# Kernel optimization log

Hardware: AMD Instinct MI355X
Metric: run time of the kernel (lower is better)

The kernel has to match this reference:

```python
import jax, jax.numpy as jnp
import numpy as np

B, S, HID = 2, 2048, 2048
H, D = 16, 128
BASE = 10000.0
NEG = -1e9


def _rope_tables(seq_len, dim, dtype):
    inv_freq = 1.0 / (BASE ** (jnp.arange(0, dim, 2, dtype=jnp.float32) / dim))
    pos = jnp.arange(seq_len, dtype=jnp.float32)
    freqs = jnp.einsum('s,d->sd', pos, inv_freq)          # [S, D/2]
    emb = jnp.concatenate([freqs, freqs], axis=-1)        # [S, D]
    return jnp.cos(emb).astype(dtype), jnp.sin(emb).astype(dtype)


def _rotate_half(x):
    x1, x2 = jnp.split(x, 2, axis=-1)
    return jnp.concatenate([-x2, x1], axis=-1)


def setup_inputs() -> dict:
    key = jax.random.key(0)
    k1, k2, k3 = jax.random.split(key, 3)
    x = jax.random.normal(k1, (B, S, HID), dtype=jnp.float32)
    w_qkv = jax.random.normal(k2, (HID, 3 * HID), dtype=jnp.float32) * (HID ** -0.5)
    w_out = jax.random.normal(k3, (HID, HID), dtype=jnp.float32) * (HID ** -0.5)
    return {"x": x, "w_qkv": w_qkv, "w_out": w_out}


def reference(x, w_qkv, w_out):
    b, s, _ = x.shape
    qkv = x @ w_qkv                                        # [B, S, 3*HID]
    qkv = qkv.reshape(b, s, 3, H, D).transpose(2, 0, 3, 1, 4)  # [3, B, H, S, D]
    q, k, v = qkv[0], qkv[1], qkv[2]
    cos, sin = _rope_tables(s, D, x.dtype)                 # [S, D]
    cos = cos[None, None]
    sin = sin[None, None]
    q = q * cos + _rotate_half(q) * sin
    k = k * cos + _rotate_half(k) * sin
    scale = 1.0 / np.sqrt(D)
    scores = jnp.einsum('bhqd,bhkd->bhqk', q, k) * scale   # [B, H, S, S]
    causal = jnp.triu(jnp.ones((s, s), dtype=bool), k=1)
    scores = jnp.where(causal[None, None], NEG, scores)
    attn = jax.nn.softmax(scores, axis=-1)
    out = jnp.einsum('bhqk,bhkd->bhqd', attn, v)           # [B, H, S, D]
    out = out.transpose(0, 2, 1, 3).reshape(b, s, H * D)
    return out @ w_out
```

## Files before the change

kernel.cpp:

```cpp
#include <hip/hip_runtime.h>
#include <hip/hip_bf16.h>

#define S_LEN 2048
#define HID_DIM 2048
#define NH 16
#define HD 128
#define N3 6144

typedef __bf16 bf16x8 __attribute__((ext_vector_type(8)));
typedef float f32x4 __attribute__((ext_vector_type(4)));
typedef float f32x16 __attribute__((ext_vector_type(16)));

#define MFMA16(a, b, c) __builtin_amdgcn_mfma_f32_16x16x32_bf16(a, b, c, 0, 0, 0)
#define MFMA32(a, b, c) __builtin_amdgcn_mfma_f32_32x32x16_bf16(a, b, c, 0, 0, 0)

__device__ __forceinline__ unsigned short f2bf(float f) {
  union { float f; unsigned u; } v; v.f = f;
  return (unsigned short)((v.u + 0x7fffu + ((v.u >> 16) & 1u)) >> 16);
}
__device__ __forceinline__ float bf2f(unsigned short h) {
  union { unsigned u; float f; } v; v.u = ((unsigned)h) << 16; return v.f;
}
__device__ __forceinline__ unsigned packbf2(float lo, float hi) {
  union { __hip_bfloat162 h2; unsigned u; } cv;
  cv.h2 = __float22bfloat162_rn(make_float2(lo, hi));
  return cv.u;
}
__device__ __forceinline__ void store_c(float* p, float v) { *p = v; }
__device__ __forceinline__ void store_c(unsigned short* p, float v) { *p = f2bf(v); }

__device__ __forceinline__ void async16(const void* g, void* l) {
  __builtin_amdgcn_global_load_lds((const __attribute__((address_space(1))) unsigned int*)g,
                                   (__attribute__((address_space(3))) unsigned int*)l,
                                   16, 0, 0);
}

__global__ __launch_bounds__(256) void cast_bf16(const float4* __restrict__ src,
                                                 ushort4* __restrict__ dst) {
  int i = blockIdx.x * 256 + threadIdx.x;
  float4 v = src[i];
  ushort4 o;
  o.x = f2bf(v.x); o.y = f2bf(v.y); o.z = f2bf(v.z); o.w = f2bf(v.w);
  dst[i] = o;
}

__global__ __launch_bounds__(256) void transpose_cast(const float* __restrict__ src,
                                                      unsigned short* __restrict__ dst,
                                                      int R, int Ccols) {
  __shared__ float t[32][33];
  int ct = Ccols >> 5;
  int bx = blockIdx.x % ct, by = blockIdx.x / ct;
  int c0 = bx << 5, r0 = by << 5;
  int lx = threadIdx.x & 31, ly = threadIdx.x >> 5;
#pragma unroll
  for (int i = 0; i < 32; i += 8)
    t[ly + i][lx] = src[(long long)(r0 + ly + i) * Ccols + c0 + lx];
  __syncthreads();
#pragma unroll
  for (int i = 0; i < 32; i += 8)
    dst[(long long)(c0 + ly + i) * R + r0 + lx] = f2bf(t[lx][ly + i]);
}

__global__ __launch_bounds__(256) void rope_tables(float* __restrict__ cosT,
                                                   float* __restrict__ sinT) {
  int idx = blockIdx.x * 256 + threadIdx.x;
  int s = idx >> 6, i = idx & 63;
  float invf = powf(10000.0f, -(float)i * (1.0f / 64.0f));
  float a = (float)s * invf;
  cosT[idx] = cosf(a);
  sinT[idx] = sinf(a);
}

template <int BM, int BN, int WM, int WN, typename OutT>
__global__ __launch_bounds__(512) void gemm_pipe(const unsigned short* __restrict__ A,
                                                 const unsigned short* __restrict__ Bt,
                                                 OutT* __restrict__ C,
                                                 int Mdim, int Ndim, int Kdim) {
  constexpr int WTM = BM / WM, WTN = BN / WN;
  constexpr int MREP = WTM / 16, NREP = WTN / 16;
  constexpr int AEL = BM * 64;
  constexpr int BEL = BN * 64;
  constexpr int BUFE = AEL + BEL;
  __shared__ unsigned short smem[2 * BUFE];

  const int ntn = Ndim / BN;
  const int nwg = (Mdim / BM) * ntn;
  int bid = blockIdx.x;
  bid = (bid & 7) * (nwg >> 3) + (bid >> 3);
  const int tm = (bid / ntn) * BM;
  const int tn = (bid % ntn) * BN;

  const int tid = threadIdx.x;
  const int w = tid >> 6, l = tid & 63;
  const int g = l >> 4, cc = l & 15;
  const int wm = w / WN, wn = w % WN;

  const int srow = tid >> 3;
  const int schunk = (tid & 7) ^ (srow & 7);
  const unsigned short* gA = A + (long long)(tm + srow) * Kdim + schunk * 8;
  const unsigned short* gB = Bt + (long long)(tn + srow) * Kdim + schunk * 8;

  const int ch0 = ((g) ^ (cc & 7)) << 3;
  const int ch1 = ((4 + g) ^ (cc & 7)) << 3;

  f32x4 acc[MREP][NREP] = {};
  bf16x8 a[MREP / 2][2], b[NREP][2];

  const int nk = Kdim >> 6;

#pragma unroll
  for (int s = 0; s < BM / 64; ++s)
    async16(gA + (long long)s * 64 * Kdim, smem + s * 4096 + w * 512);
#pragma unroll
  for (int s = 0; s < BN / 64; ++s)
    async16(gB + (long long)s * 64 * Kdim, smem + AEL + s * 4096 + w * 512);
  asm volatile("s_waitcnt vmcnt(0)" ::: "memory");
  __builtin_amdgcn_s_barrier();

  for (int kt = 0; kt < nk; ++kt) {
    const int buf = kt & 1;
    const unsigned short* Ab = smem + buf * BUFE + (wm * WTM) * 64;
    const unsigned short* Bb = smem + buf * BUFE + AEL + (wn * WTN) * 64;
    const long long kb = (long long)(kt + 1) << 6;
    unsigned short* nb = smem + (buf ^ 1) * BUFE;

#pragma unroll
    for (int i = 0; i < MREP / 2; ++i) {
      const int r = (i * 16 + cc) << 6;
      a[i][0] = *(const bf16x8*)(Ab + r + ch0);
      a[i][1] = *(const bf16x8*)(Ab + r + ch1);
    }
#pragma unroll
    for (int j = 0; j < NREP; ++j) {
      const int r = (j * 16 + cc) << 6;
      b[j][0] = *(const bf16x8*)(Bb + r + ch0);
      b[j][1] = *(const bf16x8*)(Bb + r + ch1);
    }
    if (kt + 1 < nk) {
#pragma unroll
      for (int s = 0; s < BM / 64; ++s)
        async16(gA + (long long)s * 64 * Kdim + kb, nb + s * 4096 + w * 512);
    }
    __builtin_amdgcn_s_barrier();
    __builtin_amdgcn_s_setprio(1);
#pragma unroll
    for (int i = 0; i < MREP / 2; ++i)
#pragma unroll
      for (int j = 0; j < NREP / 2; ++j) {
        acc[i][j] = MFMA16(a[i][0], b[j][0], acc[i][j]);
        acc[i][j] = MFMA16(a[i][1], b[j][1], acc[i][j]);
      }
    __builtin_amdgcn_s_setprio(0);
    __builtin_amdgcn_s_barrier();

    if (kt + 1 < nk) {
#pragma unroll
      for (int s = 0; s < BN / 64; ++s)
        async16(gB + (long long)s * 64 * Kdim + kb, nb + AEL + s * 4096 + w * 512);
    }
    __builtin_amdgcn_s_barrier();
    __builtin_amdgcn_s_setprio(1);
#pragma unroll
    for (int i = 0; i < MREP / 2; ++i)
#pragma unroll
      for (int j = 0; j < NREP / 2; ++j) {
        acc[i][NREP / 2 + j] = MFMA16(a[i][0], b[NREP / 2 + j][0], acc[i][NREP / 2 + j]);
        acc[i][NREP / 2 + j] = MFMA16(a[i][1], b[NREP / 2 + j][1], acc[i][NREP / 2 + j]);
      }
    __builtin_amdgcn_s_setprio(0);
    __builtin_amdgcn_s_barrier();

#pragma unroll
    for (int i = 0; i < MREP / 2; ++i) {
      const int r = ((WTM / 2) + i * 16 + cc) << 6;
      a[i][0] = *(const bf16x8*)(Ab + r + ch0);
      a[i][1] = *(const bf16x8*)(Ab + r + ch1);
    }
    __builtin_amdgcn_s_barrier();
    __builtin_amdgcn_s_setprio(1);
#pragma unroll
    for (int i = 0; i < MREP / 2; ++i)
#pragma unroll
      for (int j = 0; j < NREP / 2; ++j) {
        acc[MREP / 2 + i][j] = MFMA16(a[i][0], b[j][0], acc[MREP / 2 + i][j]);
        acc[MREP / 2 + i][j] = MFMA16(a[i][1], b[j][1], acc[MREP / 2 + i][j]);
      }
    __builtin_amdgcn_s_setprio(0);
    __builtin_amdgcn_s_barrier();

    __builtin_amdgcn_s_setprio(1);
#pragma unroll
    for (int i = 0; i < MREP / 2; ++i)
#pragma unroll
      for (int j = 0; j < NREP / 2; ++j) {
        acc[MREP / 2 + i][NREP / 2 + j] =
            MFMA16(a[i][0], b[NREP / 2 + j][0], acc[MREP / 2 + i][NREP / 2 + j]);
        acc[MREP / 2 + i][NREP / 2 + j] =
            MFMA16(a[i][1], b[NREP / 2 + j][1], acc[MREP / 2 + i][NREP / 2 + j]);
      }
    __builtin_amdgcn_s_setprio(0);
    asm volatile("s_waitcnt vmcnt(0)" ::: "memory");
    __builtin_amdgcn_s_barrier();
  }

  const int crow0 = tm + wm * WTM;
  const int ccol0 = tn + wn * WTN;
#pragma unroll
  for (int i = 0; i < MREP; ++i)
#pragma unroll
    for (int j = 0; j < NREP; ++j)
#pragma unroll
      for (int p = 0; p < 4; ++p) {
        int row = crow0 + i * 16 + (g << 2) + p;
        int col = ccol0 + j * 16 + cc;
        store_c(&C[(long long)row * Ndim + col], acc[i][j][p]);
      }
}

__global__ __launch_bounds__(256) void split_rope(const unsigned short* __restrict__ qkv,
                                                  const float* __restrict__ cosT,
                                                  const float* __restrict__ sinT,
                                                  unsigned short* __restrict__ Qb,
                                                  unsigned short* __restrict__ Kb,
                                                  unsigned short* __restrict__ Vt) {
  __shared__ unsigned short vtile[32][128];
  const int bid = blockIdx.x;
  const int st = bid & 63;
  const int h = (bid >> 6) & 15;
  const int b = bid >> 10;
  const int s0 = st << 5;
  const int t = threadIdx.x;
  const int d = t & 127;
  const int sl0 = t >> 7;
  const int dh = d & 63;
  const float sgn = (d < 64) ? -1.0f : 1.0f;
  const float qscale = 0.08838834764831845f;
#pragma unroll
  for (int it = 0; it < 16; ++it) {
    const int sl = sl0 + (it << 1);
    const int s = s0 + sl;
    const long long rb = ((long long)(b * S_LEN + s)) * N3 + h * HD;
    const float cv = cosT[(s << 6) + dh];
    const float sv = sinT[(s << 6) + dh];
    float qv = bf2f(qkv[rb + d]);
    float qo = bf2f(qkv[rb + (d ^ 64)]);
    float kv = bf2f(qkv[rb + HID_DIM + d]);
    float ko = bf2f(qkv[rb + HID_DIM + (d ^ 64)]);
    const long long ob = ((long long)((b * NH + h) * S_LEN + s)) * HD + d;
    Qb[ob] = f2bf((qv * cv + sgn * qo * sv) * qscale);
    Kb[ob] = f2bf(kv * cv + sgn * ko * sv);
    vtile[sl][d] = qkv[rb + 2 * HID_DIM + d];
  }
  __syncthreads();
  const int dr = t >> 1;
  const int sh = (t & 1) << 4;
  unsigned short tv[16];
#pragma unroll
  for (int j = 0; j < 16; ++j) tv[j] = vtile[sh + j][dr];
  uint4 u0, u1;
  u0.x = (unsigned)tv[0] | ((unsigned)tv[1] << 16);
  u0.y = (unsigned)tv[2] | ((unsigned)tv[3] << 16);
  u0.z = (unsigned)tv[4] | ((unsigned)tv[5] << 16);
  u0.w = (unsigned)tv[6] | ((unsigned)tv[7] << 16);
  u1.x = (unsigned)tv[8] | ((unsigned)tv[9] << 16);
  u1.y = (unsigned)tv[10] | ((unsigned)tv[11] << 16);
  u1.z = (unsigned)tv[12] | ((unsigned)tv[13] << 16);
  u1.w = (unsigned)tv[14] | ((unsigned)tv[15] << 16);
  const long long vb = ((long long)((b * NH + h) * HD + dr)) * S_LEN + s0 + sh;
  *(uint4*)(Vt + vb) = u0;
  *(uint4*)(Vt + vb + 8) = u1;
}

__global__ __launch_bounds__(256) void flash_attn(const unsigned short* __restrict__ Qg,
                                                  const unsigned short* __restrict__ Kg,
                                                  const unsigned short* __restrict__ Vt,
                                                  unsigned short* __restrict__ Ob) {
  __shared__ unsigned short smem[32768];
  const int id = blockIdx.x;
  const int bh = id & 31;
  const int qtr = (id >> 5) & 7;
  const int qt = (id >> 8) ? qtr : 15 - qtr;
  const int Q0 = qt << 7;
  const int b = bh >> 4, h = bh & 15;
  const long long base = (long long)bh * (S_LEN * HD);
  const int tid = threadIdx.x, w = tid >> 6, l = tid & 63;
  const int hi = l >> 5, q = l & 31;
  const int q0w = Q0 + (w << 5);
  const int g = l >> 4, c = l & 15;

  bf16x8 qf[8];
  {
    const unsigned short* qp = Qg + base + (long long)(q0w + q) * HD + (hi << 3);
#pragma unroll
    for (int s = 0; s < 8; ++s) qf[s] = *(const bf16x8*)(qp + (s << 4));
  }

  f32x16 oacc[4] = {};
  float m = -1e30f, lsum = 0.f;

  const int nt = (qt << 1) + 2;

  auto STAGE = [&](int kv0, int buf) {
    unsigned short* ks = smem + buf * 8192;
    unsigned short* vs = smem + 16384 + buf * 8192;
#pragma unroll
    for (int j = 0; j < 4; ++j) {
      int row = (w << 4) + (j << 2) + g;
      int chunk = c ^ (row & 7);
      async16(Kg + base + (long long)(kv0 + row) * HD + (chunk << 3),
              ks + (((w << 4) + (j << 2)) << 7));
    }
#pragma unroll
    for (int j = 0; j < 4; ++j) {
      int dr = (w << 5) + (j << 3) + (l >> 3);
      int chunk = (l & 7) ^ (dr & 7);
      async16(Vt + base + (long long)dr * S_LEN + kv0 + (chunk << 3),
              vs + (((w << 5) + (j << 3)) << 6));
    }
  };

  STAGE(0, 0);
  __syncthreads();

  int cur = 0;
  for (int t = 0; t < nt; ++t) {
    const int kv0 = t << 6;
    if (t + 1 < nt) STAGE((t + 1) << 6, cur ^ 1);

    if (kv0 < q0w + 32) {
      const unsigned short* ks = smem + cur * 8192;
      const unsigned short* vs = smem + 16384 + cur * 8192;

      f32x16 sa[2] = {};
#pragma unroll
      for (int h2 = 0; h2 < 2; ++h2) {
        const char* kb = (const char*)ks + (((h2 << 5) + q) << 8);
        const int r7 = q & 7;
#pragma unroll
        for (int s = 0; s < 8; ++s) {
          bf16x8 kf = *(const bf16x8*)(kb + ((((s << 1) + hi) ^ r7) << 4));
          sa[h2] = MFMA32(kf, qf[s], sa[h2]);
        }
      }

      if (kv0 + 63 > q0w) {
        const int qq = q0w + q;
#pragma unroll
        for (int h2 = 0; h2 < 2; ++h2)
#pragma unroll
          for (int j = 0; j < 16; ++j) {
            int kv = kv0 + (h2 << 5) + (j & 3) + ((j >> 2) << 3) + (hi << 2);
            if (kv > qq) sa[h2][j] = -1e30f;
          }
      }

      float tmax = -1e30f;
#pragma unroll
      for (int h2 = 0; h2 < 2; ++h2)
#pragma unroll
        for (int j = 0; j < 16; ++j) tmax = fmaxf(tmax, sa[h2][j]);
      tmax = fmaxf(tmax, __shfl_xor(tmax, 32));
      float mn = fmaxf(m, tmax);
      float fsc = __expf(m - mn);
      m = mn;
      float ps = 0.f;
#pragma unroll
      for (int h2 = 0; h2 < 2; ++h2)
#pragma unroll
        for (int j = 0; j < 16; ++j) {
          float pv = __expf(sa[h2][j] - mn);
          sa[h2][j] = pv;
          ps += pv;
        }
      ps += __shfl_xor(ps, 32);
      lsum = lsum * fsc + ps;
#pragma unroll
      for (int db = 0; db < 4; ++db)
#pragma unroll
        for (int j = 0; j < 16; ++j) oacc[db][j] *= fsc;

      unsigned up[2][8], wp[2][8];
#pragma unroll
      for (int h2 = 0; h2 < 2; ++h2)
#pragma unroll
        for (int k = 0; k < 8; ++k)
          up[h2][k] = packbf2(sa[h2][2 * k], sa[h2][2 * k + 1]);
#pragma unroll
      for (int h2 = 0; h2 < 2; ++h2)
#pragma unroll
        for (int k = 0; k < 8; ++k)
          wp[h2][k] = __shfl_xor((int)up[h2][k], 32);
      union Frag { unsigned u[4]; bf16x8 v; } pf[4];
#pragma unroll
      for (int s = 0; s < 4; ++s) {
        int h2 = s >> 1, q4 = (s & 1) << 2;
        pf[s].u[0] = hi ? wp[h2][q4 + 2] : up[h2][q4];
        pf[s].u[1] = hi ? wp[h2][q4 + 3] : up[h2][q4 + 1];
        pf[s].u[2] = hi ? up[h2][q4 + 2] : wp[h2][q4];
        pf[s].u[3] = hi ? up[h2][q4 + 3] : wp[h2][q4 + 1];
      }

#pragma unroll
      for (int db = 0; db < 4; ++db) {
        const char* vb = (const char*)vs + (((db << 5) + q) << 7);
        const int d7 = q & 7;
#pragma unroll
        for (int s = 0; s < 4; ++s) {
          bf16x8 vf = *(const bf16x8*)(vb + ((((s << 1) + hi) ^ d7) << 4));
          oacc[db] = MFMA32(vf, pf[s].v, oacc[db]);
        }
      }
    }

    __syncthreads();
    cur ^= 1;
  }

  const float rl = 1.0f / lsum;
#pragma unroll
  for (int db = 0; db < 4; ++db)
#pragma unroll
    for (int jg = 0; jg < 4; ++jg) {
      int d = (db << 5) + (jg << 3) + (hi << 2);
      unsigned v0 = packbf2(oacc[db][4 * jg] * rl, oacc[db][4 * jg + 1] * rl);
      unsigned v1 = packbf2(oacc[db][4 * jg + 2] * rl, oacc[db][4 * jg + 3] * rl);
      *(uint2*)(smem + (((w << 5) + q) << 7) + d) = make_uint2(v0, v1);
    }
  __syncthreads();
  {
    const int qr = tid >> 1;
    const int dh = (tid & 1) << 6;
    const uint4* src = (const uint4*)(smem + (qr << 7) + dh);
    uint4* dst = (uint4*)(Ob + (long long)((b << 11) + Q0 + qr) * HID_DIM + (h << 7) + dh);
#pragma unroll
    for (int cc2 = 0; cc2 < 8; ++cc2) dst[cc2] = src[cc2];
  }
}

extern "C" void kernel_launch(void* const* d_in, const int* in_sizes, int n_in,
                              void* d_out, int out_size, void* d_ws, size_t ws_size,
                              hipStream_t stream) {
  (void)in_sizes; (void)n_in; (void)out_size; (void)ws_size;
  const float* x = (const float*)d_in[0];
  const float* w_qkv = (const float*)d_in[1];
  const float* w_out = (const float*)d_in[2];
  float* out = (float*)d_out;
  char* ws = (char*)d_ws;

  unsigned short* xb    = (unsigned short*)(ws);
  unsigned short* wqkvT = (unsigned short*)(ws + 16777216);
  unsigned short* woutT = (unsigned short*)(ws + 41943040);
  unsigned short* qkv   = (unsigned short*)(ws + 50331648);
  unsigned short* Qb    = (unsigned short*)(ws + 100663296);
  unsigned short* Kb    = (unsigned short*)(ws + 117440512);
  unsigned short* Vt    = (unsigned short*)(ws + 134217728);
  float* cosT = (float*)(ws + 150994944);
  float* sinT = (float*)(ws + 151519232);
  unsigned short* Ob = qkv;

  cast_bf16<<<8192, 256, 0, stream>>>((const float4*)x, (ushort4*)xb);
  transpose_cast<<<12288, 256, 0, stream>>>(w_qkv, wqkvT, 2048, 6144);
  transpose_cast<<<4096, 256, 0, stream>>>(w_out, woutT, 2048, 2048);
  rope_tables<<<512, 256, 0, stream>>>(cosT, sinT);
  gemm_pipe<256, 256, 2, 4, unsigned short><<<384, 512, 0, stream>>>(xb, wqkvT, qkv, 4096, 6144, 2048);
  split_rope<<<2048, 256, 0, stream>>>(qkv, cosT, sinT, Qb, Kb, Vt);
  flash_attn<<<512, 256, 0, stream>>>(Qb, Kb, Vt, Ob);
  gemm_pipe<256, 128, 4, 2, float><<<256, 512, 0, stream>>>(Ob, woutT, out, 4096, 2048, 2048);
}
```

Before: 297.2 us.

## Deepen GEMM prefetch pipeline with split staging and partial vmcnt waits

Restructures the double-buffered GEMM so loads for tile k+2 are issued in halves interleaved between MFMA phases, and the loop waits with a partial vmcnt instead of draining all outstanding loads. This is meant to keep global-to-LDS transfers in flight across iterations and hide memory latency. The output projection GEMM also switches from a 256x128 tile with a 4x2 warp grid to a 128x256 tile with a fixed 2x4 grid. The design depends on exact vmcnt counts matching the number of issued instructions, and on correct buffer reuse ordering, which adds correctness risk.

```diff
diff --git a/kernel.cpp b/kernel.cpp
--- a/kernel.cpp
+++ b/kernel.cpp
@@ -34,6 +34,11 @@
                                    (__attribute__((address_space(3))) unsigned int*)l,
                                    16, 0, 0);
 }
+
+template <int N> __device__ __forceinline__ void vmcnt();
+template <> __device__ __forceinline__ void vmcnt<0>() { asm volatile("s_waitcnt vmcnt(0)" ::: "memory"); }
+template <> __device__ __forceinline__ void vmcnt<5>() { asm volatile("s_waitcnt vmcnt(5)" ::: "memory"); }
+template <> __device__ __forceinline__ void vmcnt<6>() { asm volatile("s_waitcnt vmcnt(6)" ::: "memory"); }
 
 __global__ __launch_bounds__(256) void cast_bf16(const float4* __restrict__ src,
                                                  ushort4* __restrict__ dst) {
@@ -71,16 +76,17 @@
   sinT[idx] = sinf(a);
 }
 
-template <int BM, int BN, int WM, int WN, typename OutT>
-__global__ __launch_bounds__(512) void gemm_pipe(const unsigned short* __restrict__ A,
-                                                 const unsigned short* __restrict__ Bt,
-                                                 OutT* __restrict__ C,
-                                                 int Mdim, int Ndim, int Kdim) {
-  constexpr int WTM = BM / WM, WTN = BN / WN;
+template <int BM, int BN, typename OutT>
+__global__ __launch_bounds__(512) void gemm_pipe8(const unsigned short* __restrict__ A,
+                                                  const unsigned short* __restrict__ Bt,
+                                                  OutT* __restrict__ C,
+                                                  int Mdim, int Ndim, int Kdim) {
+  constexpr int WTM = BM / 2, WTN = BN / 4;
   constexpr int MREP = WTM / 16, NREP = WTN / 16;
-  constexpr int AEL = BM * 64;
-  constexpr int BEL = BN * 64;
-  constexpr int BUFE = AEL + BEL;
+  constexpr int AEL = BM * 64, BEL = BN * 64, BUFE = AEL + BEL;
+  constexpr int AINST = BM / 64, BINST = BN / 64;
+  constexpr int AHALF = BM / 128, BHALF = BN / 128;
+  constexpr int VN = BN / 64 + BM / 128;
   __shared__ unsigned short smem[2 * BUFE];
 
   const int ntn = Ndim / BN;
@@ -93,7 +99,7 @@
   const int tid = threadIdx.x;
   const int w = tid >> 6, l = tid & 63;
   const int g = l >> 4, cc = l & 15;
-  const int wm = w / WN, wn = w % WN;
+  const int wm = w >> 2, wn = w & 3;
 
   const int srow = tid >> 3;
   const int schunk = (tid & 7) ^ (srow & 7);
@@ -108,21 +114,28 @@
 
   const int nk = Kdim >> 6;
 
-#pragma unroll
-  for (int s = 0; s < BM / 64; ++s)
-    async16(gA + (long long)s * 64 * Kdim, smem + s * 4096 + w * 512);
-#pragma unroll
-  for (int s = 0; s < BN / 64; ++s)
-    async16(gB + (long long)s * 64 * Kdim, smem + AEL + s * 4096 + w * 512);
-  asm volatile("s_waitcnt vmcnt(0)" ::: "memory");
+#define STAGE_A(kt2, s) \
+  async16(gA + (long long)(s) * 64 * Kdim + ((long long)(kt2) << 6), \
+          smem + ((kt2) & 1) * BUFE + (s) * 4096 + w * 512)
+#define STAGE_B(kt2, s) \
+  async16(gB + (long long)(s) * 64 * Kdim + ((long long)(kt2) << 6), \
+          smem + ((kt2) & 1) * BUFE + AEL + (s) * 4096 + w * 512)
+
+#pragma unroll
+  for (int s = 0; s < AINST; ++s) STAGE_A(0, s);
+#pragma unroll
+  for (int s = 0; s < BINST; ++s) STAGE_B(0, s);
+#pragma unroll
+  for (int s = 0; s < BINST; ++s) STAGE_B(1, s);
+#pragma unroll
+  for (int s = 0; s < AHALF; ++s) STAGE_A(1, s);
+  vmcnt<VN>();
   __builtin_amdgcn_s_barrier();
 
   for (int kt = 0; kt < nk; ++kt) {
     const int buf = kt & 1;
     const unsigned short* Ab = smem + buf * BUFE + (wm * WTM) * 64;
     const unsigned short* Bb = smem + buf * BUFE + AEL + (wn * WTN) * 64;
-    const long long kb = (long long)(kt + 1) << 6;
-    unsigned short* nb = smem + (buf ^ 1) * BUFE;
 
 #pragma unroll
     for (int i = 0; i < MREP / 2; ++i) {
@@ -138,8 +151,7 @@
     }
     if (kt + 1 < nk) {
 #pragma unroll
-      for (int s = 0; s < BM / 64; ++s)
-        async16(gA + (long long)s * 64 * Kdim + kb, nb + s * 4096 + w * 512);
+      for (int s = AHALF; s < AINST; ++s) STAGE_A(kt + 1, s);
     }
     __builtin_amdgcn_s_barrier();
     __builtin_amdgcn_s_setprio(1);
@@ -153,10 +165,9 @@
     __builtin_amdgcn_s_setprio(0);
     __builtin_amdgcn_s_barrier();
 
-    if (kt + 1 < nk) {
-#pragma unroll
-      for (int s = 0; s < BN / 64; ++s)
-        async16(gB + (long long)s * 64 * Kdim + kb, nb + AEL + s * 4096 + w * 512);
+    if (kt + 2 < nk) {
+#pragma unroll
+      for (int s = 0; s < BHALF; ++s) STAGE_B(kt + 2, s);
     }
     __builtin_amdgcn_s_barrier();
     __builtin_amdgcn_s_setprio(1);
@@ -164,8 +175,9 @@
     for (int i = 0; i < MREP / 2; ++i)
 #pragma unroll
       for (int j = 0; j < NREP / 2; ++j) {
-        acc[i][NREP / 2 + j] = MFMA16(a[i][0], b[NREP / 2 + j][0], acc[i][NREP / 2 + j]);
-        acc[i][NREP / 2 + j] = MFMA16(a[i][1], b[NREP / 2 + j][1], acc[i][NREP / 2 + j]);
+        f32x4& ac = acc[i][NREP / 2 + j];
+        ac = MFMA16(a[i][0], b[NREP / 2 + j][0], ac);
+        ac = MFMA16(a[i][1], b[NREP / 2 + j][1], ac);
       }
     __builtin_amdgcn_s_setprio(0);
     __builtin_amdgcn_s_barrier();
@@ -176,32 +188,43 @@
       a[i][0] = *(const bf16x8*)(Ab + r + ch0);
       a[i][1] = *(const bf16x8*)(Ab + r + ch1);
     }
+    if (kt + 2 < nk) {
+#pragma unroll
+      for (int s = BHALF; s < BINST; ++s) STAGE_B(kt + 2, s);
+    }
     __builtin_amdgcn_s_barrier();
     __builtin_amdgcn_s_setprio(1);
 #pragma unroll
     for (int i = 0; i < MREP / 2; ++i)
 #pragma unroll
       for (int j = 0; j < NREP / 2; ++j) {
-        acc[MREP / 2 + i][j] = MFMA16(a[i][0], b[j][0], acc[MREP / 2 + i][j]);
-        acc[MREP / 2 + i][j] = MFMA16(a[i][1], b[j][1], acc[MREP / 2 + i][j]);
+        f32x4& ac = acc[MREP / 2 + i][j];
+        ac = MFMA16(a[i][0], b[j][0], ac);
+        ac = MFMA16(a[i][1], b[j][1], ac);
       }
     __builtin_amdgcn_s_setprio(0);
     __builtin_amdgcn_s_barrier();
 
+    if (kt + 2 < nk) {
+#pragma unroll
+      for (int s = 0; s < AHALF; ++s) STAGE_A(kt + 2, s);
+    }
+    __builtin_amdgcn_s_barrier();
     __builtin_amdgcn_s_setprio(1);
 #pragma unroll
     for (int i = 0; i < MREP / 2; ++i)
 #pragma unroll
       for (int j = 0; j < NREP / 2; ++j) {
-        acc[MREP / 2 + i][NREP / 2 + j] =
-            MFMA16(a[i][0], b[NREP / 2 + j][0], acc[MREP / 2 + i][NREP / 2 + j]);
-        acc[MREP / 2 + i][NREP / 2 + j] =
-            MFMA16(a[i][1], b[NREP / 2 + j][1], acc[MREP / 2 + i][NREP / 2 + j]);
+        f32x4& ac = acc[MREP / 2 + i][NREP / 2 + j];
+        ac = MFMA16(a[i][0], b[NREP / 2 + j][0], ac);
+        ac = MFMA16(a[i][1], b[NREP / 2 + j][1], ac);
       }
     __builtin_amdgcn_s_setprio(0);
-    asm volatile("s_waitcnt vmcnt(0)" ::: "memory");
+    if (kt + 2 < nk) vmcnt<VN>(); else vmcnt<0>();
     __builtin_amdgcn_s_barrier();
   }
+#undef STAGE_A
+#undef STAGE_B
 
   const int crow0 = tm + wm * WTM;
   const int ccol0 = tn + wn * WTN;
@@ -462,8 +485,8 @@
   transpose_cast<<<12288, 256, 0, stream>>>(w_qkv, wqkvT, 2048, 6144);
   transpose_cast<<<4096, 256, 0, stream>>>(w_out, woutT, 2048, 2048);
   rope_tables<<<512, 256, 0, stream>>>(cosT, sinT);
-  gemm_pipe<256, 256, 2, 4, unsigned short><<<384, 512, 0, stream>>>(xb, wqkvT, qkv, 4096, 6144, 2048);
+  gemm_pipe8<256, 256, unsigned short><<<384, 512, 0, stream>>>(xb, wqkvT, qkv, 4096, 6144, 2048);
   split_rope<<<2048, 256, 0, stream>>>(qkv, cosT, sinT, Qb, Kb, Vt);
   flash_attn<<<512, 256, 0, stream>>>(Qb, Kb, Vt, Ob);
-  gemm_pipe<256, 128, 4, 2, float><<<256, 512, 0, stream>>>(Ob, woutT, out, 4096, 2048, 2048);
-}
+  gemm_pipe8<128, 256, float><<<256, 512, 0, stream>>>(Ob, woutT, out, 4096, 2048, 2048);
+}
```

After: 298.8 us. No clear change (+0.5%).
